# Performance work log

Hardware: AMD Instinct MI355X
Metric: run time of the kernel (lower is better)

The kernel has to match this reference:

```python
import jax, jax.numpy as jnp
import numpy as np

B = 10      # number of interacting objects
NDIM = 2    # self.n: position/velocity dimensionality

# Edge list equivalent to rel_rec/rel_send one-hot matrices (edges grouped by receiver)
_rec_idx, _send_idx = np.where(~np.eye(B, dtype=bool))


def _mlp(x, W0, b0, W1, b1, W2, b2):
    # MLP with 2 hidden softplus layers, linear output
    h = jax.nn.softplus(x @ W0 + b0)
    h = jax.nn.softplus(h @ W1 + b1)
    return h @ W2 + b2


def setup_inputs() -> dict:
    key = jax.random.key(0)
    ks = jax.random.split(key, 7)
    N = 8192            # trajectories per batch
    H = 128             # hidden width of self-dynamics MLP
    Hi = 128            # hidden width of interaction MLP
    nin = 2 * NDIM      # self MLP input dim (pos+vel)
    nout = 2 * NDIM     # n_f_out for order=1
    nin_i = 3 * NDIM    # interaction MLP input dim (p1-p2, v1, v2)
    w = lambda k, shp: jax.random.normal(k, shp, jnp.float32) / np.float32(np.sqrt(shp[0]))
    return {
        "z": jax.random.normal(ks[0], (N * B, 2 * NDIM), jnp.float32),
        "fW0": w(ks[1], (nin, H)),   "fb0": jnp.zeros((H,), jnp.float32),
        "fW1": w(ks[2], (H, H)),     "fb1": jnp.zeros((H,), jnp.float32),
        "fW2": w(ks[3], (H, nout)),  "fb2": jnp.zeros((nout,), jnp.float32),
        "iW0": w(ks[4], (nin_i, Hi)),"ib0": jnp.zeros((Hi,), jnp.float32),
        "iW1": w(ks[5], (Hi, Hi)),   "ib1": jnp.zeros((Hi,), jnp.float32),
        "iW2": w(ks[6], (Hi, nout)), "ib2": jnp.zeros((nout,), jnp.float32),
    }


def reference(z, fW0, fb0, fW1, fb1, fW2, fb2, iW0, ib0, iW1, ib1, iW2, ib2):
    # One evaluation of the ODE vector field (order=1, n_aug_dyn=n_aug_st=0).
    n = NDIM
    NB = z.shape[0]
    N = NB // B
    dz_self = _mlp(z, fW0, fb0, fW1, fb1, fW2, fb2)            # [N*B, 2n]
    z3 = z.reshape(N, B, 2 * n)
    recv = z3[:, _rec_idx]                                     # [N, B(B-1), 2n] gather (node2edge)
    send = z3[:, _send_idx]
    # odefint input: (p_recv - p_send, v_recv, v_send)  -> [N, B(B-1), 3n]
    inp = jnp.concatenate([recv[..., :n] - send[..., :n], recv[..., n:], send[..., n:]], -1)
    dz_int = _mlp(inp, iW0, ib0, iW1, ib1, iW2, ib2)           # [N, B(B-1), 2n]
    dz_int = dz_int.reshape(N, B, B - 1, 2 * n).sum(2)         # sum over senders per receiver
    dz = dz_self.reshape(N, B, 2 * n) + dz_int
    return dz.reshape(NB, 2 * n)
```

## Files before the change

kernel.cpp:

```cpp
#include <hip/hip_runtime.h>
#include <hip/hip_bf16.h>

#define NDIM 2
#define BB 10
#define H 128
#define PAIRS 90
#define ROWS 112
#define LDH 136

typedef short short8 __attribute__((ext_vector_type(8)));
typedef float floatx4 __attribute__((ext_vector_type(4)));

__device__ inline short f2bf(float x) {
    unsigned u = __float_as_uint(x);
    return (short)((u + 0x7fffu + ((u >> 16) & 1u)) >> 16);
}

#if __has_builtin(__builtin_amdgcn_cvt_pk_bf16_f32)
typedef __bf16 bf16x2_t __attribute__((ext_vector_type(2)));
__device__ inline unsigned pk2(float a, float b) {
    bf16x2_t v = __builtin_amdgcn_cvt_pk_bf16_f32(a, b);
    return __builtin_bit_cast(unsigned, v);
}
#else
__device__ inline unsigned pk2(float a, float b) {
    unsigned ua = __float_as_uint(a), ub = __float_as_uint(b);
    ua = (ua + 0x7fffu + ((ua >> 16) & 1u)) >> 16;
    ub = (ub + 0x7fffu + ((ub >> 16) & 1u)) & 0xffff0000u;
    return ua | ub;
}
#endif

__device__ inline float softplus(float x) {
#if __has_builtin(__builtin_amdgcn_exp2f) && __has_builtin(__builtin_amdgcn_logf)
    float t = __builtin_amdgcn_exp2f(-fabsf(x) * 1.4426950408889634f);
    return fmaf(__builtin_amdgcn_logf(1.f + t), 0.6931471805599453f, fmaxf(x, 0.f));
#else
    return fmaxf(x, 0.f) + __logf(1.f + __expf(-fabsf(x)));
#endif
}

__global__ void prep_weights(const float* __restrict__ iW1, const float* __restrict__ fW1,
                             const float* __restrict__ iW2, const float* __restrict__ fW2,
                             short* __restrict__ W1Fi, short* __restrict__ W1Ff,
                             short* __restrict__ W2Fi, short* __restrict__ W2Ff) {
    int t = blockIdx.x * blockDim.x + threadIdx.x;
    int stride = gridDim.x * blockDim.x;
    for (int fidx = t; fidx < 16384; fidx += stride) {
        int j = fidx & 7, lane = (fidx >> 3) & 63, nt = (fidx >> 9) & 7, ks = fidx >> 12;
        int k = 32 * ks + ((lane >> 4) << 3) + j;
        int n = 16 * nt + (lane & 15);
        W1Fi[fidx] = f2bf(iW1[k * H + n]);
        W1Ff[fidx] = f2bf(fW1[k * H + n]);
    }
    for (int fidx = t; fidx < 2048; fidx += stride) {
        int j = fidx & 7, lane = (fidx >> 3) & 63, ks = fidx >> 9;
        int k = 32 * ks + ((lane >> 4) << 3) + j;
        int n = lane & 15;
        W2Fi[fidx] = (n < 4) ? f2bf(iW2[k * 4 + n]) : (short)0;
        W2Ff[fidx] = (n < 4) ? f2bf(fW2[k * 4 + n]) : (short)0;
    }
}

__global__ __launch_bounds__(256) void fused_kernel(
    const float* __restrict__ z,
    const float* __restrict__ iW0, const float* __restrict__ ib0,
    const float* __restrict__ ib1, const float* __restrict__ ib2,
    const float* __restrict__ fW0, const float* __restrict__ fb0,
    const float* __restrict__ fb1, const float* __restrict__ fb2,
    const short* __restrict__ W1Fi, const short* __restrict__ W2Fi,
    const short* __restrict__ W1Ff, const short* __restrict__ W2Ff,
    float* __restrict__ out) {
    __shared__ __align__(16) short h0s[ROWS * LDH];
    __shared__ __align__(16) float uws[2560];
    __shared__ __align__(16) float4 zs4[BB];
    float* us   = uws;
    float* wss  = uws + 1280;
    float* outs = uws;

    int n = blockIdx.x;
    int tid = threadIdx.x, lane = tid & 63, wave = tid >> 6;
    int rit = lane & 15, quad = lane >> 4;

    short8 w1i[2][4], w2i[4], w2s[4];
#pragma unroll
    for (int q = 0; q < 2; ++q) {
        int nt = 2 * wave + q;
#pragma unroll
        for (int ks = 0; ks < 4; ++ks)
            w1i[q][ks] = *(const short8*)(W1Fi + ((ks * 8 + nt) * 64 + lane) * 8);
    }
#pragma unroll
    for (int ks = 0; ks < 4; ++ks) {
        w2i[ks] = *(const short8*)(W2Fi + (ks * 64 + lane) * 8);
        w2s[ks] = *(const short8*)(W2Ff + (ks * 64 + lane) * 8);
    }

    if (tid < BB) zs4[tid] = ((const float4*)z)[n * BB + tid];
    __syncthreads();

    {
        int c = tid & 127;
        float iw0 = iW0[c], iw1 = iW0[128 + c], iw2 = iW0[256 + c], iw3 = iW0[384 + c];
        float iw4 = iW0[512 + c], iw5 = iW0[640 + c];
        float ib = ib0[c];
        int b0 = tid >> 7;
#pragma unroll
        for (int t = 0; t < 5; ++t) {
            int b = b0 + 2 * t;
            float4 zb = zs4[b];
            us[b * 128 + c]  = ib + zb.x * iw0 + zb.y * iw1 + zb.z * iw2 + zb.w * iw3;
            wss[b * 128 + c] = -zb.x * iw0 - zb.y * iw1 + zb.z * iw4 + zb.w * iw5;
        }
    }
#pragma unroll
    for (int t = 0; t < 3; ++t) {
        int u = tid + t * 256;
        if (u < 640) {
            int b = u >> 6, c2 = (u & 63) * 2;
            float4 zb = zs4[b];
            float2 w0 = *(const float2*)(fW0 + c2);
            float2 w1 = *(const float2*)(fW0 + 128 + c2);
            float2 w2 = *(const float2*)(fW0 + 256 + c2);
            float2 w3 = *(const float2*)(fW0 + 384 + c2);
            float2 bb = *(const float2*)(fb0 + c2);
            float a0 = bb.x + zb.x * w0.x + zb.y * w1.x + zb.z * w2.x + zb.w * w3.x;
            float a1 = bb.y + zb.x * w0.y + zb.y * w1.y + zb.z * w2.y + zb.w * w3.y;
            *(unsigned*)(h0s + (96 + b) * LDH + c2) = pk2(softplus(a0), softplus(a1));
        }
    }
    if (tid < 192) {
        int r = 106 + (tid >> 5), kk = (tid & 31) * 4;
        *(uint2*)(h0s + r * LDH + kk) = uint2{0u, 0u};
    }
    __syncthreads();

#pragma unroll
    for (int t = 0; t < 12; ++t) {
        int u = tid + t * 256;
        int m = u >> 5, kk = (u & 31) << 2;
        uint2 pk = {0u, 0u};
        if (m < PAIRS) {
            int i = (m * 57) >> 9;
            int s = m - 9 * i;
            int j = s + (s >= i);
            float4 uu = *(float4*)(us + i * 128 + kk);
            float4 ww = *(float4*)(wss + j * 128 + kk);
            pk.x = pk2(softplus(uu.x + ww.x), softplus(uu.y + ww.y));
            pk.y = pk2(softplus(uu.z + ww.z), softplus(uu.w + ww.w));
        }
        *(uint2*)(h0s + m * LDH + kk) = pk;
    }
    __syncthreads();

    floatx4 acc[2][7];
    floatx4 zz = {0.f, 0.f, 0.f, 0.f};
#pragma unroll
    for (int q = 0; q < 2; ++q)
#pragma unroll
        for (int mt = 0; mt < 7; ++mt) acc[q][mt] = zz;
#pragma unroll
    for (int ks = 0; ks < 4; ++ks) {
        short8 bf[7];
#pragma unroll
        for (int mt = 0; mt < 7; ++mt)
            bf[mt] = *(const short8*)(h0s + (16 * mt + rit) * LDH + 32 * ks + quad * 8);
        short8 fa0 = *(const short8*)(W1Ff + ((ks * 8 + 2 * wave) * 64 + lane) * 8);
        short8 fa1 = *(const short8*)(W1Ff + ((ks * 8 + 2 * wave + 1) * 64 + lane) * 8);
#pragma unroll
        for (int mt = 0; mt < 6; ++mt) {
            acc[0][mt] = __builtin_amdgcn_mfma_f32_16x16x32_bf16(w1i[0][ks], bf[mt], acc[0][mt], 0, 0, 0);
            acc[1][mt] = __builtin_amdgcn_mfma_f32_16x16x32_bf16(w1i[1][ks], bf[mt], acc[1][mt], 0, 0, 0);
        }
        acc[0][6] = __builtin_amdgcn_mfma_f32_16x16x32_bf16(fa0, bf[6], acc[0][6], 0, 0, 0);
        acc[1][6] = __builtin_amdgcn_mfma_f32_16x16x32_bf16(fa1, bf[6], acc[1][6], 0, 0, 0);
    }
    __syncthreads();

#pragma unroll
    for (int q = 0; q < 2; ++q) {
        int nt = 2 * wave + q;
        float4 bi = *(const float4*)(ib1 + 16 * nt + 4 * quad);
        float4 bs = *(const float4*)(fb1 + 16 * nt + 4 * quad);
#pragma unroll
        for (int mt = 0; mt < 7; ++mt) {
            float4 bb = (mt == 6) ? bs : bi;
            floatx4 a = acc[q][mt];
            uint2 pk;
            pk.x = pk2(softplus(a[0] + bb.x), softplus(a[1] + bb.y));
            pk.y = pk2(softplus(a[2] + bb.z), softplus(a[3] + bb.w));
            *(uint2*)(h0s + (16 * mt + rit) * LDH + 16 * nt + 4 * quad) = pk;
        }
    }
    __syncthreads();

    for (int mt = wave; mt < 7; mt += 4) {
        floatx4 a = zz;
        if (mt == 6) {
#pragma unroll
            for (int ks = 0; ks < 4; ++ks) {
                short8 bf = *(const short8*)(h0s + (16 * mt + rit) * LDH + 32 * ks + quad * 8);
                a = __builtin_amdgcn_mfma_f32_16x16x32_bf16(w2s[ks], bf, a, 0, 0, 0);
            }
            if (quad == 0) {
                float4 bb = *(const float4*)(fb2);
                float4 o = {a[0] + bb.x, a[1] + bb.y, a[2] + bb.z, a[3] + bb.w};
                *(float4*)(outs + (16 * mt + rit) * 4) = o;
            }
        } else {
#pragma unroll
            for (int ks = 0; ks < 4; ++ks) {
                short8 bf = *(const short8*)(h0s + (16 * mt + rit) * LDH + 32 * ks + quad * 8);
                a = __builtin_amdgcn_mfma_f32_16x16x32_bf16(w2i[ks], bf, a, 0, 0, 0);
            }
            if (quad == 0) {
                float4 bb = *(const float4*)(ib2);
                float4 o = {a[0] + bb.x, a[1] + bb.y, a[2] + bb.z, a[3] + bb.w};
                *(float4*)(outs + (16 * mt + rit) * 4) = o;
            }
        }
    }
    __syncthreads();

    if (tid < BB * 4) {
        int i = tid >> 2, c = tid & 3;
        float s = outs[(96 + i) * 4 + c];
#pragma unroll
        for (int p = 0; p < 9; ++p) s += outs[(9 * i + p) * 4 + c];
        out[(n * BB + i) * 4 + c] = s;
    }
}

extern "C" void kernel_launch(void* const* d_in, const int* in_sizes, int n_in,
                              void* d_out, int out_size, void* d_ws, size_t ws_size,
                              hipStream_t stream) {
    const float* z   = (const float*)d_in[0];
    const float* fW0 = (const float*)d_in[1];
    const float* fb0 = (const float*)d_in[2];
    const float* fW1 = (const float*)d_in[3];
    const float* fb1 = (const float*)d_in[4];
    const float* fW2 = (const float*)d_in[5];
    const float* fb2 = (const float*)d_in[6];
    const float* iW0 = (const float*)d_in[7];
    const float* ib0 = (const float*)d_in[8];
    const float* iW1 = (const float*)d_in[9];
    const float* ib1 = (const float*)d_in[10];
    const float* iW2 = (const float*)d_in[11];
    const float* ib2 = (const float*)d_in[12];
    float* out = (float*)d_out;

    short* ws = (short*)d_ws;
    short* W1Fi = ws;
    short* W1Ff = ws + 16384;
    short* W2Fi = ws + 32768;
    short* W2Ff = ws + 34816;

    int NB = in_sizes[0] / (2 * NDIM);
    int Nsys = NB / BB;

    hipLaunchKernelGGL(prep_weights, dim3(64), dim3(256), 0, stream,
                       iW1, fW1, iW2, fW2, W1Fi, W1Ff, W2Fi, W2Ff);
    hipLaunchKernelGGL(fused_kernel, dim3(Nsys), dim3(256), 0, stream,
                       z, iW0, ib0, ib1, ib2, fW0, fb0, fb1, fb2,
                       W1Fi, W2Fi, W1Ff, W2Ff, out);
}
```

Before: 207.8 us.

## Use 512-thread blocks, fold log2e into weights, simplify softplus

Doubles the block to 8 waves so each wave owns one 16-column tile of layer 1 and one row tile of layer 2, which halves per-wave accumulators and weight registers. The log2(e) factor is folded into the layer-0/1 weights and biases, and layer-1 biases are preloaded into the accumulators, so softplus becomes exp2 then log2 with no abs/max/scale. Dropping the max(x,0)+log(1+exp(-|x|)) form risks overflow or precision loss for large positive pre-activations, where exp2 can reach infinity.

```diff
diff --git a/kernel.cpp b/kernel.cpp
--- a/kernel.cpp
+++ b/kernel.cpp
@@ -7,6 +7,8 @@
 #define PAIRS 90
 #define ROWS 112
 #define LDH 136
+#define LOG2E 1.4426950408889634f
+#define LN2   0.6931471805599453f
 
 typedef short short8 __attribute__((ext_vector_type(8)));
 typedef float floatx4 __attribute__((ext_vector_type(4)));
@@ -31,27 +33,29 @@
 }
 #endif
 
-__device__ inline float softplus(float x) {
+__device__ inline float sp2(float xs) {
 #if __has_builtin(__builtin_amdgcn_exp2f) && __has_builtin(__builtin_amdgcn_logf)
-    float t = __builtin_amdgcn_exp2f(-fabsf(x) * 1.4426950408889634f);
-    return fmaf(__builtin_amdgcn_logf(1.f + t), 0.6931471805599453f, fmaxf(x, 0.f));
+    float t = __builtin_amdgcn_exp2f(xs);
+    return __builtin_amdgcn_logf(1.f + t) * LN2;
 #else
-    return fmaxf(x, 0.f) + __logf(1.f + __expf(-fabsf(x)));
+    return log2f(1.f + exp2f(xs)) * LN2;
 #endif
 }
 
 __global__ void prep_weights(const float* __restrict__ iW1, const float* __restrict__ fW1,
                              const float* __restrict__ iW2, const float* __restrict__ fW2,
+                             const float* __restrict__ ib1, const float* __restrict__ fb1,
                              short* __restrict__ W1Fi, short* __restrict__ W1Ff,
-                             short* __restrict__ W2Fi, short* __restrict__ W2Ff) {
+                             short* __restrict__ W2Fi, short* __restrict__ W2Ff,
+                             float* __restrict__ ib1s, float* __restrict__ fb1s) {
     int t = blockIdx.x * blockDim.x + threadIdx.x;
     int stride = gridDim.x * blockDim.x;
     for (int fidx = t; fidx < 16384; fidx += stride) {
         int j = fidx & 7, lane = (fidx >> 3) & 63, nt = (fidx >> 9) & 7, ks = fidx >> 12;
         int k = 32 * ks + ((lane >> 4) << 3) + j;
         int n = 16 * nt + (lane & 15);
-        W1Fi[fidx] = f2bf(iW1[k * H + n]);
-        W1Ff[fidx] = f2bf(fW1[k * H + n]);
+        W1Fi[fidx] = f2bf(iW1[k * H + n] * LOG2E);
+        W1Ff[fidx] = f2bf(fW1[k * H + n] * LOG2E);
     }
     for (int fidx = t; fidx < 2048; fidx += stride) {
         int j = fidx & 7, lane = (fidx >> 3) & 63, ks = fidx >> 9;
@@ -60,16 +64,21 @@
         W2Fi[fidx] = (n < 4) ? f2bf(iW2[k * 4 + n]) : (short)0;
         W2Ff[fidx] = (n < 4) ? f2bf(fW2[k * 4 + n]) : (short)0;
     }
-}
-
-__global__ __launch_bounds__(256) void fused_kernel(
+    if (t < 128) {
+        ib1s[t] = ib1[t] * LOG2E;
+        fb1s[t] = fb1[t] * LOG2E;
+    }
+}
+
+__global__ __launch_bounds__(512, 4) void fused_kernel(
     const float* __restrict__ z,
     const float* __restrict__ iW0, const float* __restrict__ ib0,
-    const float* __restrict__ ib1, const float* __restrict__ ib2,
+    const float* __restrict__ ib2,
     const float* __restrict__ fW0, const float* __restrict__ fb0,
-    const float* __restrict__ fb1, const float* __restrict__ fb2,
+    const float* __restrict__ fb2,
     const short* __restrict__ W1Fi, const short* __restrict__ W2Fi,
     const short* __restrict__ W1Ff, const short* __restrict__ W2Ff,
+    const float* __restrict__ ib1s, const float* __restrict__ fb1s,
     float* __restrict__ out) {
     __shared__ __align__(16) short h0s[ROWS * LDH];
     __shared__ __align__(16) float uws[2560];
@@ -81,19 +90,13 @@
     int n = blockIdx.x;
     int tid = threadIdx.x, lane = tid & 63, wave = tid >> 6;
     int rit = lane & 15, quad = lane >> 4;
-
-    short8 w1i[2][4], w2i[4], w2s[4];
-#pragma unroll
-    for (int q = 0; q < 2; ++q) {
-        int nt = 2 * wave + q;
-#pragma unroll
-        for (int ks = 0; ks < 4; ++ks)
-            w1i[q][ks] = *(const short8*)(W1Fi + ((ks * 8 + nt) * 64 + lane) * 8);
-    }
+    int nt = wave;
+
+    short8 w1[4], fa[4];
 #pragma unroll
     for (int ks = 0; ks < 4; ++ks) {
-        w2i[ks] = *(const short8*)(W2Fi + (ks * 64 + lane) * 8);
-        w2s[ks] = *(const short8*)(W2Ff + (ks * 64 + lane) * 8);
+        w1[ks] = *(const short8*)(W1Fi + ((ks * 8 + nt) * 64 + lane) * 8);
+        fa[ks] = *(const short8*)(W1Ff + ((ks * 8 + nt) * 64 + lane) * 8);
     }
 
     if (tid < BB) zs4[tid] = ((const float4*)z)[n * BB + tid];
@@ -101,32 +104,35 @@
 
     {
         int c = tid & 127;
-        float iw0 = iW0[c], iw1 = iW0[128 + c], iw2 = iW0[256 + c], iw3 = iW0[384 + c];
-        float iw4 = iW0[512 + c], iw5 = iW0[640 + c];
-        float ib = ib0[c];
+        float iw0 = iW0[c] * LOG2E, iw1 = iW0[128 + c] * LOG2E;
+        float iw2 = iW0[256 + c] * LOG2E, iw3 = iW0[384 + c] * LOG2E;
+        float iw4 = iW0[512 + c] * LOG2E, iw5 = iW0[640 + c] * LOG2E;
+        float ib = ib0[c] * LOG2E;
         int b0 = tid >> 7;
 #pragma unroll
-        for (int t = 0; t < 5; ++t) {
-            int b = b0 + 2 * t;
-            float4 zb = zs4[b];
-            us[b * 128 + c]  = ib + zb.x * iw0 + zb.y * iw1 + zb.z * iw2 + zb.w * iw3;
-            wss[b * 128 + c] = -zb.x * iw0 - zb.y * iw1 + zb.z * iw4 + zb.w * iw5;
-        }
-    }
-#pragma unroll
-    for (int t = 0; t < 3; ++t) {
-        int u = tid + t * 256;
+        for (int t = 0; t < 3; ++t) {
+            int b = b0 + 4 * t;
+            if (b < BB) {
+                float4 zb = zs4[b];
+                us[b * 128 + c]  = ib + zb.x * iw0 + zb.y * iw1 + zb.z * iw2 + zb.w * iw3;
+                wss[b * 128 + c] = -zb.x * iw0 - zb.y * iw1 + zb.z * iw4 + zb.w * iw5;
+            }
+        }
+    }
+#pragma unroll
+    for (int t = 0; t < 2; ++t) {
+        int u = tid + 512 * t;
         if (u < 640) {
             int b = u >> 6, c2 = (u & 63) * 2;
             float4 zb = zs4[b];
             float2 w0 = *(const float2*)(fW0 + c2);
-            float2 w1 = *(const float2*)(fW0 + 128 + c2);
-            float2 w2 = *(const float2*)(fW0 + 256 + c2);
+            float2 w1_ = *(const float2*)(fW0 + 128 + c2);
+            float2 w2_ = *(const float2*)(fW0 + 256 + c2);
             float2 w3 = *(const float2*)(fW0 + 384 + c2);
             float2 bb = *(const float2*)(fb0 + c2);
-            float a0 = bb.x + zb.x * w0.x + zb.y * w1.x + zb.z * w2.x + zb.w * w3.x;
-            float a1 = bb.y + zb.x * w0.y + zb.y * w1.y + zb.z * w2.y + zb.w * w3.y;
-            *(unsigned*)(h0s + (96 + b) * LDH + c2) = pk2(softplus(a0), softplus(a1));
+            float a0 = bb.x + zb.x * w0.x + zb.y * w1_.x + zb.z * w2_.x + zb.w * w3.x;
+            float a1 = bb.y + zb.x * w0.y + zb.y * w1_.y + zb.z * w2_.y + zb.w * w3.y;
+            *(unsigned*)(h0s + (96 + b) * LDH + c2) = pk2(sp2(a0 * LOG2E), sp2(a1 * LOG2E));
         }
     }
     if (tid < 192) {
@@ -135,89 +141,76 @@
     }
     __syncthreads();
 
-#pragma unroll
-    for (int t = 0; t < 12; ++t) {
-        int u = tid + t * 256;
-        int m = u >> 5, kk = (u & 31) << 2;
-        uint2 pk = {0u, 0u};
-        if (m < PAIRS) {
-            int i = (m * 57) >> 9;
-            int s = m - 9 * i;
-            int j = s + (s >= i);
-            float4 uu = *(float4*)(us + i * 128 + kk);
-            float4 ww = *(float4*)(wss + j * 128 + kk);
-            pk.x = pk2(softplus(uu.x + ww.x), softplus(uu.y + ww.y));
-            pk.y = pk2(softplus(uu.z + ww.z), softplus(uu.w + ww.w));
-        }
-        *(uint2*)(h0s + m * LDH + kk) = pk;
-    }
-    __syncthreads();
-
-    floatx4 acc[2][7];
-    floatx4 zz = {0.f, 0.f, 0.f, 0.f};
-#pragma unroll
-    for (int q = 0; q < 2; ++q)
-#pragma unroll
-        for (int mt = 0; mt < 7; ++mt) acc[q][mt] = zz;
+    {
+        int kk = (tid & 31) << 2;
+        int m0 = tid >> 5;
+#pragma unroll
+        for (int t = 0; t < 6; ++t) {
+            int m = m0 + 16 * t;
+            uint2 pk = {0u, 0u};
+            if (m < PAIRS) {
+                int i = (m * 57) >> 9;
+                int s = m - 9 * i;
+                int j = s + (s >= i);
+                float4 uu = *(float4*)(us + i * 128 + kk);
+                float4 ww = *(float4*)(wss + j * 128 + kk);
+                pk.x = pk2(sp2(uu.x + ww.x), sp2(uu.y + ww.y));
+                pk.y = pk2(sp2(uu.z + ww.z), sp2(uu.w + ww.w));
+            }
+            *(uint2*)(h0s + m * LDH + kk) = pk;
+        }
+    }
+    __syncthreads();
+
+    float4 bi = *(const float4*)(ib1s + 16 * nt + 4 * quad);
+    float4 bs = *(const float4*)(fb1s + 16 * nt + 4 * quad);
+    floatx4 acc[7];
+#pragma unroll
+    for (int mt = 0; mt < 6; ++mt) acc[mt] = floatx4{bi.x, bi.y, bi.z, bi.w};
+    acc[6] = floatx4{bs.x, bs.y, bs.z, bs.w};
 #pragma unroll
     for (int ks = 0; ks < 4; ++ks) {
         short8 bf[7];
 #pragma unroll
         for (int mt = 0; mt < 7; ++mt)
             bf[mt] = *(const short8*)(h0s + (16 * mt + rit) * LDH + 32 * ks + quad * 8);
-        short8 fa0 = *(const short8*)(W1Ff + ((ks * 8 + 2 * wave) * 64 + lane) * 8);
-        short8 fa1 = *(const short8*)(W1Ff + ((ks * 8 + 2 * wave + 1) * 64 + lane) * 8);
-#pragma unroll
-        for (int mt = 0; mt < 6; ++mt) {
-            acc[0][mt] = __builtin_amdgcn_mfma_f32_16x16x32_bf16(w1i[0][ks], bf[mt], acc[0][mt], 0, 0, 0);
-            acc[1][mt] = __builtin_amdgcn_mfma_f32_16x16x32_bf16(w1i[1][ks], bf[mt], acc[1][mt], 0, 0, 0);
-        }
-        acc[0][6] = __builtin_amdgcn_mfma_f32_16x16x32_bf16(fa0, bf[6], acc[0][6], 0, 0, 0);
-        acc[1][6] = __builtin_amdgcn_mfma_f32_16x16x32_bf16(fa1, bf[6], acc[1][6], 0, 0, 0);
-    }
-    __syncthreads();
-
-#pragma unroll
-    for (int q = 0; q < 2; ++q) {
-        int nt = 2 * wave + q;
-        float4 bi = *(const float4*)(ib1 + 16 * nt + 4 * quad);
-        float4 bs = *(const float4*)(fb1 + 16 * nt + 4 * quad);
-#pragma unroll
-        for (int mt = 0; mt < 7; ++mt) {
-            float4 bb = (mt == 6) ? bs : bi;
-            floatx4 a = acc[q][mt];
-            uint2 pk;
-            pk.x = pk2(softplus(a[0] + bb.x), softplus(a[1] + bb.y));
-            pk.y = pk2(softplus(a[2] + bb.z), softplus(a[3] + bb.w));
-            *(uint2*)(h0s + (16 * mt + rit) * LDH + 16 * nt + 4 * quad) = pk;
-        }
-    }
-    __syncthreads();
-
-    for (int mt = wave; mt < 7; mt += 4) {
-        floatx4 a = zz;
-        if (mt == 6) {
-#pragma unroll
-            for (int ks = 0; ks < 4; ++ks) {
-                short8 bf = *(const short8*)(h0s + (16 * mt + rit) * LDH + 32 * ks + quad * 8);
-                a = __builtin_amdgcn_mfma_f32_16x16x32_bf16(w2s[ks], bf, a, 0, 0, 0);
-            }
-            if (quad == 0) {
-                float4 bb = *(const float4*)(fb2);
-                float4 o = {a[0] + bb.x, a[1] + bb.y, a[2] + bb.z, a[3] + bb.w};
-                *(float4*)(outs + (16 * mt + rit) * 4) = o;
-            }
-        } else {
-#pragma unroll
-            for (int ks = 0; ks < 4; ++ks) {
-                short8 bf = *(const short8*)(h0s + (16 * mt + rit) * LDH + 32 * ks + quad * 8);
-                a = __builtin_amdgcn_mfma_f32_16x16x32_bf16(w2i[ks], bf, a, 0, 0, 0);
-            }
-            if (quad == 0) {
-                float4 bb = *(const float4*)(ib2);
-                float4 o = {a[0] + bb.x, a[1] + bb.y, a[2] + bb.z, a[3] + bb.w};
-                *(float4*)(outs + (16 * mt + rit) * 4) = o;
-            }
+#pragma unroll
+        for (int mt = 0; mt < 6; ++mt)
+            acc[mt] = __builtin_amdgcn_mfma_f32_16x16x32_bf16(w1[ks], bf[mt], acc[mt], 0, 0, 0);
+        acc[6] = __builtin_amdgcn_mfma_f32_16x16x32_bf16(fa[ks], bf[6], acc[6], 0, 0, 0);
+    }
+    __syncthreads();
+
+#pragma unroll
+    for (int mt = 0; mt < 7; ++mt) {
+        floatx4 a = acc[mt];
+        uint2 pk;
+        pk.x = pk2(sp2(a[0]), sp2(a[1]));
+        pk.y = pk2(sp2(a[2]), sp2(a[3]));
+        *(uint2*)(h0s + (16 * mt + rit) * LDH + 16 * nt + 4 * quad) = pk;
+    }
+    __syncthreads();
+
+    if (wave < 7) {
+        const short* W2 = (wave == 6) ? W2Ff : W2Fi;
+        const float* b2 = (wave == 6) ? fb2 : ib2;
+        short8 w2[4];
+#pragma unroll
+        for (int ks = 0; ks < 4; ++ks)
+            w2[ks] = *(const short8*)(W2 + (ks * 64 + lane) * 8);
+        floatx4 a = {0.f, 0.f, 0.f, 0.f};
+        if (quad == 0) {
+            float4 bb = *(const float4*)b2;
+            a = floatx4{bb.x, bb.y, bb.z, bb.w};
+        }
+#pragma unroll
+        for (int ks = 0; ks < 4; ++ks) {
+            short8 bf = *(const short8*)(h0s + (16 * wave + rit) * LDH + 32 * ks + quad * 8);
+            a = __builtin_amdgcn_mfma_f32_16x16x32_bf16(w2[ks], bf, a, 0, 0, 0);
+        }
+        if (quad == 0) {
+            float4 o = {a[0], a[1], a[2], a[3]};
+            *(float4*)(outs + (16 * wave + rit) * 4) = o;
         }
     }
     __syncthreads();
@@ -249,18 +242,21 @@
     const float* ib2 = (const float*)d_in[12];
     float* out = (float*)d_out;
 
-    short* ws = (short*)d_ws;
-    short* W1Fi = ws;
-    short* W1Ff = ws + 16384;
-    short* W2Fi = ws + 32768;
-    short* W2Ff = ws + 34816;
+    short* wsS = (short*)d_ws;
+    short* W1Fi = wsS;
+    short* W1Ff = wsS + 16384;
+    short* W2Fi = wsS + 32768;
+    short* W2Ff = wsS + 34816;
+    float* ib1s = (float*)(wsS + 36864);
+    float* fb1s = ib1s + 128;
 
     int NB = in_sizes[0] / (2 * NDIM);
     int Nsys = NB / BB;
 
     hipLaunchKernelGGL(prep_weights, dim3(64), dim3(256), 0, stream,
-                       iW1, fW1, iW2, fW2, W1Fi, W1Ff, W2Fi, W2Ff);
-    hipLaunchKernelGGL(fused_kernel, dim3(Nsys), dim3(256), 0, stream,
-                       z, iW0, ib0, ib1, ib2, fW0, fb0, fb1, fb2,
-                       W1Fi, W2Fi, W1Ff, W2Ff, out);
-}
+                       iW1, fW1, iW2, fW2, ib1, fb1,
+                       W1Fi, W1Ff, W2Fi, W2Ff, ib1s, fb1s);
+    hipLaunchKernelGGL(fused_kernel, dim3(Nsys), dim3(512), 0, stream,
+                       z, iW0, ib0, ib2, fW0, fb0, fb2,
+                       W1Fi, W2Fi, W1Ff, W2Ff, ib1s, fb1s, out);
+}
```

Result: faster. 190.7 us (-8.2%).
